# Performance work log

Hardware: AMD Instinct MI355X
Metric: run time of the kernel (lower is better)

Reference implementation:

```python
import jax, jax.numpy as jnp
import numpy as np

B, S, D, H = 128, 512, 256, 512
N_ASSETS = 50
OUT_DIM = N_ASSETS * (N_ASSETS + 1) // 2  # 1275, lower-triangular Cholesky entries


def setup_inputs() -> dict:
    key = jax.random.key(0)
    k = jax.random.split(key, 6)
    x = jax.random.normal(k[0], (B, S, D), dtype=jnp.float32)
    # Layer 0: fused gate weights [D+H, 4H] in gate order (i, f, g, o);
    # equivalent to four separate nn.Linear(D+H, H) layers concatenated.
    W0 = jax.random.normal(k[1], (D + H, 4 * H), jnp.float32) / np.sqrt(D + H)
    b0 = jnp.zeros((4 * H,), jnp.float32).at[H:2 * H].set(1.0)  # forget bias = 1.0
    # Layer 1: input is h of layer 0 -> [H+H, 4H]
    W1 = jax.random.normal(k[2], (2 * H, 4 * H), jnp.float32) / np.sqrt(2 * H)
    b1 = jnp.zeros((4 * H,), jnp.float32).at[H:2 * H].set(1.0)
    Wp = jax.random.normal(k[3], (H, OUT_DIM), jnp.float32) / np.sqrt(H)
    bp = jnp.zeros((OUT_DIM,), jnp.float32)
    return {"x": x, "W0": W0, "b0": b0, "W1": W1, "b1": b1, "Wp": Wp, "bp": bp}


def _cell(xt, h, c, W, b):
    # combined = cat(x, h); single fused GEMM for the 4 gates
    z = jnp.concatenate([xt, h], axis=1) @ W + b  # [B, 4H]
    i, f, g, o = jnp.split(z, 4, axis=1)
    c_new = jax.nn.sigmoid(f) * c + jax.nn.sigmoid(i) * jnp.tanh(g)
    h_new = jax.nn.sigmoid(o) * jnp.tanh(c_new)
    return h_new, c_new


def reference(x, W0, b0, W1, b1, Wp, bp):
    batch = x.shape[0]
    hdim = W0.shape[1] // 4
    init = tuple(jnp.zeros((batch, hdim), x.dtype) for _ in range(4))  # h0,c0,h1,c1

    def step(carry, xt):
        h0, c0, h1, c1 = carry
        h0, c0 = _cell(xt, h0, c0, W0, b0)
        h1, c1 = _cell(h0, h1, c1, W1, b1)
        return (h0, c0, h1, c1), None

    (h0, c0, h1, c1), _ = jax.lax.scan(step, init, jnp.swapaxes(x, 0, 1))
    # Original stacks all timestep outputs but only projects the last hidden state.
    return h1 @ Wp + bp  # [B, OUT_DIM]
```

## Files before the change

kernel.cpp:

```cpp
#include <hip/hip_runtime.h>
#include <stdint.h>

#define BATCH 128
#define SEQ   512
#define DIN   256
#define HID   512
#define NWG   256
#define TPB   512
#define NSLOT 513
#define OUTD  1275
#define HSLOT (BATCH * HID)

#define WS_FLAGS 0
#define WS_H0    4096
#define WS_H1    (4096 + 524288)
#define WS_H1FIN (4096 + 524288 + 262144)
#define WS_XB    (WS_H1FIN + 262144)
#define WS_MSET  (4096 + 524288 + 262144)

typedef __attribute__((ext_vector_type(8))) short bf16x8;
typedef __attribute__((ext_vector_type(4))) unsigned int uint4v;
typedef __attribute__((ext_vector_type(4))) float f32x4;

static __device__ __forceinline__ unsigned short f2bf(float f) {
  unsigned int u = __builtin_bit_cast(unsigned int, f);
  u += 0x7FFFu + ((u >> 16) & 1u);
  return (unsigned short)(u >> 16);
}
static __device__ __forceinline__ float sigmoidf_fast(float v) {
  float e = __expf(-fabsf(v));
  float s = 1.0f / (1.0f + e);
  return v >= 0.0f ? s : 1.0f - s;
}
static __device__ __forceinline__ float tanhf_fast(float v) {
  float e = __expf(-2.0f * fabsf(v));
  float t = (1.0f - e) / (1.0f + e);
  return v >= 0.0f ? t : -t;
}

static __device__ __forceinline__ void ldg_nc(bf16x8& d, const unsigned short* p) {
  asm volatile("global_load_dwordx4 %0, %1, off sc0 sc1" : "=v"(d) : "v"(p));
}
static __device__ __forceinline__ void ldg_nc_dw(unsigned int& d, const unsigned int* p) {
  asm volatile("global_load_dword %0, %1, off sc0 sc1" : "=v"(d) : "v"(p));
}
static __device__ __forceinline__ void stg_nc16(unsigned short* p, uint4v v) {
  asm volatile("global_store_dwordx4 %0, %1, off sc0 sc1" :: "v"(p), "v"(v) : "memory");
}
static __device__ __forceinline__ void stg_nc4(unsigned int* p, unsigned int v) {
  asm volatile("global_store_dword %0, %1, off sc0 sc1" :: "v"(p), "v"(v) : "memory");
}
#define WAIT_TIE1(v) asm volatile("s_waitcnt vmcnt(0)" : "+v"(v) :: "memory")
#define WAIT_TIE4(A)                                                          \
  asm volatile("s_waitcnt vmcnt(0)"                                           \
               : "+v"((A)[0]), "+v"((A)[1]), "+v"((A)[2]), "+v"((A)[3])       \
               :: "memory")
#define WAIT_TIE6(A)                                                          \
  asm volatile("s_waitcnt vmcnt(0)"                                           \
               : "+v"((A)[0]), "+v"((A)[1]), "+v"((A)[2]), "+v"((A)[3]),      \
                 "+v"((A)[4]), "+v"((A)[5]) :: "memory")
#define WAIT_TIE8(A)                                                          \
  asm volatile("s_waitcnt vmcnt(0)"                                           \
               : "+v"((A)[0]), "+v"((A)[1]), "+v"((A)[2]), "+v"((A)[3]),      \
                 "+v"((A)[4]), "+v"((A)[5]), "+v"((A)[6]), "+v"((A)[7])       \
               :: "memory")

static __device__ __forceinline__ int poll_min32(const unsigned int* base, int thr) {
  const unsigned int* fp = base + (threadIdx.x & 31);
  for (;;) {
    unsigned int v;
    ldg_nc_dw(v, fp);
    WAIT_TIE1(v);
    if (__ballot(v >= (unsigned int)thr) == ~0ull) {
      int mn = (int)v;
#pragma unroll
      for (int o = 1; o < 64; o <<= 1) {
        int t = __shfl_xor(mn, o, 64);
        mn = t < mn ? t : mn;
      }
      return mn;
    }
    __builtin_amdgcn_s_sleep(1);
  }
}
static __device__ __forceinline__ int poll_min64(const unsigned int* base, int thr) {
  const unsigned int* fp = base + (threadIdx.x & 63);
  for (;;) {
    unsigned int v;
    ldg_nc_dw(v, fp);
    WAIT_TIE1(v);
    if (__ballot(v >= (unsigned int)thr) == ~0ull) {
      int mn = (int)v;
#pragma unroll
      for (int o = 1; o < 64; o <<= 1) {
        int t = __shfl_xor(mn, o, 64);
        mn = t < mn ? t : mn;
      }
      return mn;
    }
    __builtin_amdgcn_s_sleep(1);
  }
}

__global__ __launch_bounds__(256) void xprep(const float* __restrict__ x,
                                             unsigned short* __restrict__ xb) {
  int p = blockIdx.x;
  int lane = threadIdx.x & 63;
  int g4 = threadIdx.x >> 6;
  int c15 = lane & 15, q = lane >> 4;
  for (int g = 0; g < 16; ++g) {
    int idx = g * 4 + g4;
    int mi = idx >> 3, kt = idx & 7;
    int row = mi * 16 + c15;
    const float* src = x + ((size_t)row * SEQ + p) * DIN + kt * 32 + q * 8;
    f32x4 a = *(const f32x4*)src;
    f32x4 b = *(const f32x4*)(src + 4);
    bf16x8 v;
    v[0] = (short)f2bf(a[0]); v[1] = (short)f2bf(a[1]);
    v[2] = (short)f2bf(a[2]); v[3] = (short)f2bf(a[3]);
    v[4] = (short)f2bf(b[0]); v[5] = (short)f2bf(b[1]);
    v[6] = (short)f2bf(b[2]); v[7] = (short)f2bf(b[3]);
    *(bf16x8*)&xb[((((size_t)p * 8 + mi) * 8 + kt) * 64 + lane) * 8] = v;
  }
}

template <bool USE_XB>
__global__ __launch_bounds__(TPB, 1) void lstm_persistent(
    const float* __restrict__ x, const unsigned short* __restrict__ xb,
    const float* __restrict__ W0, const float* __restrict__ b0,
    const float* __restrict__ W1, const float* __restrict__ b1,
    unsigned int* __restrict__ flags, unsigned short* __restrict__ h0buf,
    unsigned short* __restrict__ h1buf, float* __restrict__ h1fin)
{
  __shared__ unsigned short sWf[4 * 32 * 64 * 8];
  __shared__ float red[4 * 32 * 33];
  __shared__ unsigned short stage[32 * 16];

  const int tid  = threadIdx.x;
  const int wgid = blockIdx.x;
  const int g    = wgid >> 6;
  const int r    = wgid & 63;
  const bool isA = (r < 32);
  const int unit0 = (isA ? r : r - 32) << 4;
  const int lane = tid & 63;
  const int wv   = tid >> 6;
  const int m    = wv & 1;
  const int kq   = wv >> 1;
  const int c15  = lane & 15;
  const int q    = lane >> 4;
  const int miG  = g * 2 + m;
  const int KT   = isA ? 24 : 32;

  {
    const float* W = isA ? W0 : W1;
    for (int f = tid; f < 4 * KT * 64; f += TPB) {
      int ct = f / (KT * 64);
      int rem = f - ct * (KT * 64);
      int kt = rem >> 6, ln = rem & 63;
      int qq = ln >> 4, cc = ln & 15;
      int u_local = ct * 4 + (cc >> 2);
      int gate = cc & 3;
      int gcol = gate * HID + unit0 + u_local;
      int kbase = kt * 32 + qq * 8;
      bf16x8 v;
#pragma unroll
      for (int j = 0; j < 8; ++j)
        v[j] = (short)f2bf(W[(size_t)(kbase + j) * 2048 + gcol]);
      *(bf16x8*)&sWf[(size_t)f * 8] = v;
    }
  }

  const int grow_ = tid >> 3, gu = tid & 7;
  float bias_c[2][4];
  float cst[2] = {0.f, 0.f};
  if (tid < 256) {
    const float* bv = isA ? b0 : b1;
#pragma unroll
    for (int ch = 0; ch < 2; ++ch)
#pragma unroll
      for (int gt = 0; gt < 4; ++gt)
        bias_c[ch][gt] = bv[gt * HID + unit0 + ch * 8 + gu];
  }
  __syncthreads();

  unsigned int* myflags = flags + g * 64;

#define BFRAG(ct, kt) (*(const bf16x8*)&sWf[((((ct) * KT + (kt)) << 6) + lane) << 3])

  int selfSeen = 0, bothSeen = 0, ringSeen = 0;

  for (int p = 0; p < NSLOT; ++p) {
    const unsigned short* h0rd = h0buf + (size_t)((p + 3) & 3) * HSLOT;
    unsigned short* h0wr       = h0buf + (size_t)(p & 3) * HSLOT;
    const unsigned short* h1rd = h1buf + (size_t)(p & 1) * HSLOT;
    unsigned short* h1wr       = h1buf + (size_t)((p + 1) & 1) * HSLOT;
    const bool active = isA ? (p < SEQ) : (p >= 1);

    f32x4 acc[4];
#pragma unroll
    for (int ct = 0; ct < 4; ++ct) acc[ct] = (f32x4){0.f, 0.f, 0.f, 0.f};

    if (isA && active) {
      int ktlo = kq * 6, kthi = ktlo + 6;
      for (int kt = ktlo; kt < kthi && kt < 8; ++kt) {
        bf16x8 ax;
        if (USE_XB) {
          ax = *(const bf16x8*)&xb[((((size_t)p * 8 + miG) * 8 + kt) * 64 + lane) * 8];
        } else {
          const float* xp0 = x + (((size_t)(miG * 16 + c15)) * SEQ + p) * DIN + kt * 32 + q * 8;
          f32x4 a = *(const f32x4*)xp0;
          f32x4 b = *(const f32x4*)(xp0 + 4);
          ax[0] = (short)f2bf(a[0]); ax[1] = (short)f2bf(a[1]);
          ax[2] = (short)f2bf(a[2]); ax[3] = (short)f2bf(a[3]);
          ax[4] = (short)f2bf(b[0]); ax[5] = (short)f2bf(b[1]);
          ax[6] = (short)f2bf(b[2]); ax[7] = (short)f2bf(b[3]);
        }
#pragma unroll
        for (int ct = 0; ct < 4; ++ct)
          acc[ct] = __builtin_amdgcn_mfma_f32_16x16x32_bf16(ax, BFRAG(ct, kt), acc[ct], 0, 0, 0);
      }
    }

    if (wv == 0 && p > 0) {
      if (isA) {
        if (selfSeen < p) selfSeen = poll_min32(myflags, p);
      } else {
        if (bothSeen < p) bothSeen = poll_min64(myflags, p);
      }
    }
    __syncthreads();

    if (active) {
      if (isA) {
        if (kq == 1) {
          bf16x8 ah[4];
#pragma unroll
          for (int i = 0; i < 4; ++i)
            ldg_nc(ah[i], h0rd + ((size_t)(miG * 16 + i) * 64 + lane) * 8);
          WAIT_TIE4(ah);
#pragma unroll
          for (int i = 0; i < 4; ++i)
#pragma unroll
            for (int ct = 0; ct < 4; ++ct)
              acc[ct] = __builtin_amdgcn_mfma_f32_16x16x32_bf16(ah[i], BFRAG(ct, 8 + i), acc[ct], 0, 0, 0);
        } else if (kq >= 2) {
          bf16x8 ah[6];
          int kt0 = kq * 6;
#pragma unroll
          for (int i = 0; i < 6; ++i)
            ldg_nc(ah[i], h0rd + ((size_t)(miG * 16 + (kt0 - 8 + i)) * 64 + lane) * 8);
          WAIT_TIE6(ah);
#pragma unroll
          for (int i = 0; i < 6; ++i)
#pragma unroll
            for (int ct = 0; ct < 4; ++ct)
              acc[ct] = __builtin_amdgcn_mfma_f32_16x16x32_bf16(ah[i], BFRAG(ct, kt0 + i), acc[ct], 0, 0, 0);
        }
      } else {
        bf16x8 ah[8];
        const unsigned short* src = (kq < 2) ? h0rd : h1rd;
        int ktf0 = (kq < 2) ? kq * 8 : (kq - 2) * 8;
#pragma unroll
        for (int i = 0; i < 8; ++i)
          ldg_nc(ah[i], src + ((size_t)(miG * 16 + ktf0 + i) * 64 + lane) * 8);
        WAIT_TIE8(ah);
#pragma unroll
        for (int i = 0; i < 8; ++i)
#pragma unroll
          for (int ct = 0; ct < 4; ++ct)
            acc[ct] = __builtin_amdgcn_mfma_f32_16x16x32_bf16(ah[i], BFRAG(ct, kq * 8 + i), acc[ct], 0, 0, 0);
      }
    }

#pragma unroll
    for (int ch = 0; ch < 2; ++ch) {
      __syncthreads();
      if (active) {
        int lrow = m * 16 + q * 4;
#pragma unroll
        for (int t = 0; t < 2; ++t)
#pragma unroll
          for (int rr = 0; rr < 4; ++rr)
            red[(kq * 32 + lrow + rr) * 33 + t * 16 + c15] = acc[ch * 2 + t][rr];
      }
      __syncthreads();
      if (active && tid < 256) {
        float z[4];
#pragma unroll
        for (int gt = 0; gt < 4; ++gt) {
          float s = bias_c[ch][gt];
          int cidx = gu * 4 + gt;
#pragma unroll
          for (int k2 = 0; k2 < 4; ++k2)
            s += red[(k2 * 32 + grow_) * 33 + cidx];
          z[gt] = s;
        }
        float cn = sigmoidf_fast(z[1]) * cst[ch] + sigmoidf_fast(z[0]) * tanhf_fast(z[2]);
        cst[ch] = cn;
        float hn = sigmoidf_fast(z[3]) * tanhf_fast(cn);
        stage[grow_ * 16 + ch * 8 + gu] = f2bf(hn);
        if (!isA && p == NSLOT - 1)
          h1fin[(size_t)(g * 32 + grow_) * HID + unit0 + ch * 8 + gu] = hn;
      }
    }
    __syncthreads();

    if (wv == 0) {
      if (isA && active && p > 3 && ringSeen < p - 2)
        ringSeen = poll_min32(myflags + 32, p - 2);
      if (active && tid < 64) {
        int row = tid >> 1, qq2 = tid & 1;
        uint4v v = *(const uint4v*)&stage[row * 16 + qq2 * 8];
        int mi = g * 2 + (row >> 4), r15 = row & 15;
        int ktu = unit0 >> 5;
        int qu = ((unit0 & 31) >> 3) + qq2;
        unsigned short* dst = (isA ? h0wr : h1wr) +
            ((size_t)(mi * 16 + ktu) * 64 + qu * 16 + r15) * 8;
        stg_nc16(dst, v);
      }
      asm volatile("s_waitcnt vmcnt(0)" ::: "memory");
      if (tid == 0) stg_nc4(myflags + r, (unsigned int)(p + 1));
    }
  }
#undef BFRAG
}

__global__ __launch_bounds__(256) void proj_kernel(
    const float* __restrict__ h1, const float* __restrict__ Wp,
    const float* __restrict__ bp, float* __restrict__ out)
{
  int o = blockIdx.x * 256 + threadIdx.x;
  int b = blockIdx.y;
  if (o >= OUTD) return;
  const float* hr = h1 + (size_t)b * HID;
  float acc = bp[o];
#pragma unroll 8
  for (int k = 0; k < HID; ++k)
    acc = fmaf(hr[k], Wp[(size_t)k * OUTD + o], acc);
  out[(size_t)b * OUTD + o] = acc;
}

extern "C" void kernel_launch(void* const* d_in, const int* in_sizes, int n_in,
                              void* d_out, int out_size, void* d_ws, size_t ws_size,
                              hipStream_t stream) {
  const float* x  = (const float*)d_in[0];
  const float* W0 = (const float*)d_in[1];
  const float* b0 = (const float*)d_in[2];
  const float* W1 = (const float*)d_in[3];
  const float* b1 = (const float*)d_in[4];
  const float* Wp = (const float*)d_in[5];
  const float* bp = (const float*)d_in[6];
  float* out = (float*)d_out;

  char* ws = (char*)d_ws;
  unsigned int* flags = (unsigned int*)(ws + WS_FLAGS);
  unsigned short* h0b = (unsigned short*)(ws + WS_H0);
  unsigned short* h1b = (unsigned short*)(ws + WS_H1);
  float* h1fin        = (float*)(ws + WS_H1FIN);
  unsigned short* xbp = (unsigned short*)(ws + WS_XB);
  const size_t need_xb = (size_t)WS_XB + (size_t)SEQ * BATCH * DIN * 2;
  const bool use_xb = (ws_size >= need_xb);

  hipMemsetAsync(d_ws, 0, WS_MSET, stream);
  if (use_xb) {
    hipLaunchKernelGGL(xprep, dim3(SEQ), dim3(256), 0, stream, x, xbp);
    hipLaunchKernelGGL(lstm_persistent<true>, dim3(NWG), dim3(TPB), 0, stream,
                       x, xbp, W0, b0, W1, b1, flags, h0b, h1b, h1fin);
  } else {
    hipLaunchKernelGGL(lstm_persistent<false>, dim3(NWG), dim3(TPB), 0, stream,
                       x, xbp, W0, b0, W1, b1, flags, h0b, h1b, h1fin);
  }
  hipLaunchKernelGGL(proj_kernel, dim3((OUTD + 255) / 256, BATCH), dim3(256), 0, stream,
                     h1fin, Wp, bp, out);
}
```

Baseline: 2.919 ms.

## Embed step tags in hidden-state words to replace flag-based synchronization

Hidden states are now stored as fp32 words whose low 10 mantissa bits carry the timestep tag. Consumers poll the data itself (pollcvt) until every word matches the expected step, then convert to bf16, which removes the per-step barrier, LDS staging and flag round-trip. A coarser progress counter still guards ring-buffer reuse. The cost is twice the global traffic for h, spinning on data loads, and slight precision loss from the overwritten mantissa bits.

```diff
diff --git a/kernel.cpp b/kernel.cpp
--- a/kernel.cpp
+++ b/kernel.cpp
@@ -9,17 +9,16 @@
 #define TPB   512
 #define NSLOT 513
 #define OUTD  1275
-#define HSLOT (BATCH * HID)
+#define HSLOTF (BATCH * HID)
 
 #define WS_FLAGS 0
-#define WS_H0    4096
-#define WS_H1    (4096 + 524288)
-#define WS_H1FIN (4096 + 524288 + 262144)
-#define WS_XB    (WS_H1FIN + 262144)
-#define WS_MSET  (4096 + 524288 + 262144)
+#define WS_H0R   4096
+#define WS_H1R   (4096 + 1048576)
+#define WS_H1FIN (4096 + 2097152)
+#define WS_XB    (4096 + 2097152 + 262144)
+#define WS_MSET  (4096 + 2097152)
 
 typedef __attribute__((ext_vector_type(8))) short bf16x8;
-typedef __attribute__((ext_vector_type(4))) unsigned int uint4v;
 typedef __attribute__((ext_vector_type(4))) float f32x4;
 
 static __device__ __forceinline__ unsigned short f2bf(float f) {
@@ -38,51 +37,17 @@
   return v >= 0.0f ? t : -t;
 }
 
-static __device__ __forceinline__ void ldg_nc(bf16x8& d, const unsigned short* p) {
-  asm volatile("global_load_dwordx4 %0, %1, off sc0 sc1" : "=v"(d) : "v"(p));
-}
 static __device__ __forceinline__ void ldg_nc_dw(unsigned int& d, const unsigned int* p) {
   asm volatile("global_load_dword %0, %1, off sc0 sc1" : "=v"(d) : "v"(p));
 }
-static __device__ __forceinline__ void stg_nc16(unsigned short* p, uint4v v) {
-  asm volatile("global_store_dwordx4 %0, %1, off sc0 sc1" :: "v"(p), "v"(v) : "memory");
+static __device__ __forceinline__ void ldg_nc_f4(f32x4& d, const float* p) {
+  asm volatile("global_load_dwordx4 %0, %1, off sc0 sc1" : "=v"(d) : "v"(p));
 }
 static __device__ __forceinline__ void stg_nc4(unsigned int* p, unsigned int v) {
   asm volatile("global_store_dword %0, %1, off sc0 sc1" :: "v"(p), "v"(v) : "memory");
 }
 #define WAIT_TIE1(v) asm volatile("s_waitcnt vmcnt(0)" : "+v"(v) :: "memory")
-#define WAIT_TIE4(A)                                                          \
-  asm volatile("s_waitcnt vmcnt(0)"                                           \
-               : "+v"((A)[0]), "+v"((A)[1]), "+v"((A)[2]), "+v"((A)[3])       \
-               :: "memory")
-#define WAIT_TIE6(A)                                                          \
-  asm volatile("s_waitcnt vmcnt(0)"                                           \
-               : "+v"((A)[0]), "+v"((A)[1]), "+v"((A)[2]), "+v"((A)[3]),      \
-                 "+v"((A)[4]), "+v"((A)[5]) :: "memory")
-#define WAIT_TIE8(A)                                                          \
-  asm volatile("s_waitcnt vmcnt(0)"                                           \
-               : "+v"((A)[0]), "+v"((A)[1]), "+v"((A)[2]), "+v"((A)[3]),      \
-                 "+v"((A)[4]), "+v"((A)[5]), "+v"((A)[6]), "+v"((A)[7])       \
-               :: "memory")
-
-static __device__ __forceinline__ int poll_min32(const unsigned int* base, int thr) {
-  const unsigned int* fp = base + (threadIdx.x & 31);
-  for (;;) {
-    unsigned int v;
-    ldg_nc_dw(v, fp);
-    WAIT_TIE1(v);
-    if (__ballot(v >= (unsigned int)thr) == ~0ull) {
-      int mn = (int)v;
-#pragma unroll
-      for (int o = 1; o < 64; o <<= 1) {
-        int t = __shfl_xor(mn, o, 64);
-        mn = t < mn ? t : mn;
-      }
-      return mn;
-    }
-    __builtin_amdgcn_s_sleep(1);
-  }
-}
+
 static __device__ __forceinline__ int poll_min64(const unsigned int* base, int thr) {
   const unsigned int* fp = base + (threadIdx.x & 63);
   for (;;) {
@@ -92,13 +57,84 @@
     if (__ballot(v >= (unsigned int)thr) == ~0ull) {
       int mn = (int)v;
 #pragma unroll
-      for (int o = 1; o < 64; o <<= 1) {
-        int t = __shfl_xor(mn, o, 64);
-        mn = t < mn ? t : mn;
-      }
+      for (int o = 1; o < 64; o <<= 1) { int t = __shfl_xor(mn, o, 64); mn = t < mn ? t : mn; }
       return mn;
     }
     __builtin_amdgcn_s_sleep(1);
+  }
+}
+
+template <int N>
+static __device__ __forceinline__ void pollcvt(const float* a0, const float* cb,
+                                               unsigned tgt, bf16x8* out) {
+  f32x4 lo[N], hi[N];
+  for (;;) {
+    {
+      unsigned c[N];
+#pragma unroll
+      for (int i = 0; i < N; ++i)
+        ldg_nc_dw(c[i], (const unsigned int*)(cb + (size_t)i * 512));
+      if constexpr (N == 4) {
+        asm volatile("s_waitcnt vmcnt(0)"
+          : "+v"(c[0]), "+v"(c[1]), "+v"(c[2]), "+v"(c[3]) :: "memory");
+      } else if constexpr (N == 6) {
+        asm volatile("s_waitcnt vmcnt(0)"
+          : "+v"(c[0]), "+v"(c[1]), "+v"(c[2]), "+v"(c[3]), "+v"(c[4]), "+v"(c[5])
+          :: "memory");
+      } else {
+        asm volatile("s_waitcnt vmcnt(0)"
+          : "+v"(c[0]), "+v"(c[1]), "+v"(c[2]), "+v"(c[3]),
+            "+v"(c[4]), "+v"(c[5]), "+v"(c[6]), "+v"(c[7]) :: "memory");
+      }
+      unsigned acc = 0;
+#pragma unroll
+      for (int i = 0; i < N; ++i) acc |= c[i] ^ tgt;
+      if (__ballot((acc & 1023u) == 0u) != ~0ull) {
+        __builtin_amdgcn_s_sleep(2);
+        continue;
+      }
+    }
+#pragma unroll
+    for (int i = 0; i < N; ++i) {
+      ldg_nc_f4(lo[i], a0 + (size_t)i * 512);
+      ldg_nc_f4(hi[i], a0 + (size_t)i * 512 + 4);
+    }
+    if constexpr (N == 4) {
+      asm volatile("s_waitcnt vmcnt(0)"
+        : "+v"(lo[0]), "+v"(lo[1]), "+v"(lo[2]), "+v"(lo[3]),
+          "+v"(hi[0]), "+v"(hi[1]), "+v"(hi[2]), "+v"(hi[3]) :: "memory");
+    } else if constexpr (N == 6) {
+      asm volatile("s_waitcnt vmcnt(0)"
+        : "+v"(lo[0]), "+v"(lo[1]), "+v"(lo[2]), "+v"(lo[3]), "+v"(lo[4]), "+v"(lo[5]),
+          "+v"(hi[0]), "+v"(hi[1]), "+v"(hi[2]), "+v"(hi[3]), "+v"(hi[4]), "+v"(hi[5])
+        :: "memory");
+    } else {
+      asm volatile("s_waitcnt vmcnt(0)"
+        : "+v"(lo[0]), "+v"(lo[1]), "+v"(lo[2]), "+v"(lo[3]),
+          "+v"(lo[4]), "+v"(lo[5]), "+v"(lo[6]), "+v"(lo[7]),
+          "+v"(hi[0]), "+v"(hi[1]), "+v"(hi[2]), "+v"(hi[3]),
+          "+v"(hi[4]), "+v"(hi[5]), "+v"(hi[6]), "+v"(hi[7]) :: "memory");
+    }
+    unsigned acc = 0;
+#pragma unroll
+    for (int i = 0; i < N; ++i)
+#pragma unroll
+      for (int j = 0; j < 4; ++j) {
+        acc |= __builtin_bit_cast(unsigned, lo[i][j]) ^ tgt;
+        acc |= __builtin_bit_cast(unsigned, hi[i][j]) ^ tgt;
+      }
+    if (__ballot((acc & 1023u) == 0u) == ~0ull) break;
+    __builtin_amdgcn_s_sleep(1);
+  }
+#pragma unroll
+  for (int i = 0; i < N; ++i) {
+    bf16x8 v;
+#pragma unroll
+    for (int j = 0; j < 4; ++j) {
+      v[j]     = (short)f2bf(lo[i][j]);
+      v[4 + j] = (short)f2bf(hi[i][j]);
+    }
+    out[i] = v;
   }
 }
 
@@ -129,12 +165,11 @@
     const float* __restrict__ x, const unsigned short* __restrict__ xb,
     const float* __restrict__ W0, const float* __restrict__ b0,
     const float* __restrict__ W1, const float* __restrict__ b1,
-    unsigned int* __restrict__ flags, unsigned short* __restrict__ h0buf,
-    unsigned short* __restrict__ h1buf, float* __restrict__ h1fin)
+    unsigned int* __restrict__ prog, float* __restrict__ h0r,
+    float* __restrict__ h1r, float* __restrict__ h1fin)
 {
   __shared__ unsigned short sWf[4 * 32 * 64 * 8];
   __shared__ float red[4 * 32 * 33];
-  __shared__ unsigned short stage[32 * 16];
 
   const int tid  = threadIdx.x;
   const int wgid = blockIdx.x;
@@ -173,32 +208,41 @@
   const int grow_ = tid >> 3, gu = tid & 7;
   float bias_c[2][4];
   float cst[2] = {0.f, 0.f};
+  size_t hoff[2] = {0, 0};
   if (tid < 256) {
     const float* bv = isA ? b0 : b1;
 #pragma unroll
-    for (int ch = 0; ch < 2; ++ch)
+    for (int ch = 0; ch < 2; ++ch) {
 #pragma unroll
       for (int gt = 0; gt < 4; ++gt)
         bias_c[ch][gt] = bv[gt * HID + unit0 + ch * 8 + gu];
+      int U = unit0 + ch * 8 + gu;
+      int mi = g * 2 + (grow_ >> 4), r15g = grow_ & 15;
+      hoff[ch] = ((size_t)(mi * 16 + (U >> 5)) * 64 + ((U & 31) >> 3) * 16 + r15g) * 8 + gu;
+    }
   }
   __syncthreads();
 
-  unsigned int* myflags = flags + g * 64;
+  unsigned int* progF = prog + g * 64;
 
 #define BFRAG(ct, kt) (*(const bf16x8*)&sWf[((((ct) * KT + (kt)) << 6) + lane) << 3])
 
-  int selfSeen = 0, bothSeen = 0, ringSeen = 0;
+  int guardSeen = 0;
 
   for (int p = 0; p < NSLOT; ++p) {
-    const unsigned short* h0rd = h0buf + (size_t)((p + 3) & 3) * HSLOT;
-    unsigned short* h0wr       = h0buf + (size_t)(p & 3) * HSLOT;
-    const unsigned short* h1rd = h1buf + (size_t)(p & 1) * HSLOT;
-    unsigned short* h1wr       = h1buf + (size_t)((p + 1) & 1) * HSLOT;
+    const float* h0rd = h0r + (size_t)((p + 3) & 3) * HSLOTF;
+    float*       h0wr = h0r + (size_t)(p & 3) * HSLOTF;
+    const float* h1rd = h1r + (size_t)((p + 3) & 3) * HSLOTF;
+    float*       h1wr = h1r + (size_t)(p & 3) * HSLOTF;
     const bool active = isA ? (p < SEQ) : (p >= 1);
+    const unsigned tgt = (unsigned)p;
 
     f32x4 acc[4];
 #pragma unroll
     for (int ct = 0; ct < 4; ++ct) acc[ct] = (f32x4){0.f, 0.f, 0.f, 0.f};
+
+    if (wv == 0 && p > 3 && guardSeen < p - 2)
+      guardSeen = poll_min64(progF, p - 2);
 
     if (isA && active) {
       int ktlo = kq * 6, kthi = ktlo + 6;
@@ -221,54 +265,52 @@
       }
     }
 
-    if (wv == 0 && p > 0) {
-      if (isA) {
-        if (selfSeen < p) selfSeen = poll_min32(myflags, p);
-      } else {
-        if (bothSeen < p) bothSeen = poll_min64(myflags, p);
-      }
-    }
-    __syncthreads();
-
     if (active) {
       if (isA) {
-        if (kq == 1) {
+        if (p > 0 && kq == 1) {
           bf16x8 ah[4];
-#pragma unroll
-          for (int i = 0; i < 4; ++i)
-            ldg_nc(ah[i], h0rd + ((size_t)(miG * 16 + i) * 64 + lane) * 8);
-          WAIT_TIE4(ah);
+          const float* a0 = h0rd + ((size_t)(miG * 16 + 0) * 64 + lane) * 8;
+          const float* cb = h0rd + ((size_t)(miG * 16 + 0) * 64 + q * 16) * 8;
+          pollcvt<4>(a0, cb, tgt, ah);
 #pragma unroll
           for (int i = 0; i < 4; ++i)
 #pragma unroll
             for (int ct = 0; ct < 4; ++ct)
               acc[ct] = __builtin_amdgcn_mfma_f32_16x16x32_bf16(ah[i], BFRAG(ct, 8 + i), acc[ct], 0, 0, 0);
-        } else if (kq >= 2) {
+        } else if (p > 0 && kq >= 2) {
           bf16x8 ah[6];
-          int kt0 = kq * 6;
+          int f0 = kq * 6 - 8;
+          const float* a0 = h0rd + ((size_t)(miG * 16 + f0) * 64 + lane) * 8;
+          const float* cb = h0rd + ((size_t)(miG * 16 + f0) * 64 + q * 16) * 8;
+          pollcvt<6>(a0, cb, tgt, ah);
 #pragma unroll
           for (int i = 0; i < 6; ++i)
-            ldg_nc(ah[i], h0rd + ((size_t)(miG * 16 + (kt0 - 8 + i)) * 64 + lane) * 8);
-          WAIT_TIE6(ah);
-#pragma unroll
-          for (int i = 0; i < 6; ++i)
 #pragma unroll
             for (int ct = 0; ct < 4; ++ct)
-              acc[ct] = __builtin_amdgcn_mfma_f32_16x16x32_bf16(ah[i], BFRAG(ct, kt0 + i), acc[ct], 0, 0, 0);
+              acc[ct] = __builtin_amdgcn_mfma_f32_16x16x32_bf16(ah[i], BFRAG(ct, kq * 6 + i), acc[ct], 0, 0, 0);
         }
       } else {
-        bf16x8 ah[8];
-        const unsigned short* src = (kq < 2) ? h0rd : h1rd;
-        int ktf0 = (kq < 2) ? kq * 8 : (kq - 2) * 8;
-#pragma unroll
-        for (int i = 0; i < 8; ++i)
-          ldg_nc(ah[i], src + ((size_t)(miG * 16 + ktf0 + i) * 64 + lane) * 8);
-        WAIT_TIE8(ah);
-#pragma unroll
-        for (int i = 0; i < 8; ++i)
-#pragma unroll
-          for (int ct = 0; ct < 4; ++ct)
-            acc[ct] = __builtin_amdgcn_mfma_f32_16x16x32_bf16(ah[i], BFRAG(ct, kq * 8 + i), acc[ct], 0, 0, 0);
+        if (kq < 2) {
+          bf16x8 ah[8];
+          const float* a0 = h0rd + ((size_t)(miG * 16 + kq * 8) * 64 + lane) * 8;
+          const float* cb = h0rd + ((size_t)(miG * 16 + kq * 8) * 64 + q * 16) * 8;
+          pollcvt<8>(a0, cb, tgt, ah);
+#pragma unroll
+          for (int i = 0; i < 8; ++i)
+#pragma unroll
+            for (int ct = 0; ct < 4; ++ct)
+              acc[ct] = __builtin_amdgcn_mfma_f32_16x16x32_bf16(ah[i], BFRAG(ct, kq * 8 + i), acc[ct], 0, 0, 0);
+        } else if (p > 1) {
+          bf16x8 ah[8];
+          const float* a0 = h1rd + ((size_t)(miG * 16 + (kq - 2) * 8) * 64 + lane) * 8;
+          const float* cb = h1rd + ((size_t)(miG * 16 + (kq - 2) * 8) * 64 + q * 16) * 8;
+          pollcvt<8>(a0, cb, tgt, ah);
+#pragma unroll
+          for (int i = 0; i < 8; ++i)
+#pragma unroll
+            for (int ct = 0; ct < 4; ++ct)
+              acc[ct] = __builtin_amdgcn_mfma_f32_16x16x32_bf16(ah[i], BFRAG(ct, kq * 8 + i), acc[ct], 0, 0, 0);
+        }
       }
     }
 
@@ -298,29 +340,14 @@
         float cn = sigmoidf_fast(z[1]) * cst[ch] + sigmoidf_fast(z[0]) * tanhf_fast(z[2]);
         cst[ch] = cn;
         float hn = sigmoidf_fast(z[3]) * tanhf_fast(cn);
-        stage[grow_ * 16 + ch * 8 + gu] = f2bf(hn);
+        unsigned hb = (__builtin_bit_cast(unsigned, hn) & ~1023u) | (unsigned)(p + 1);
+        stg_nc4((unsigned int*)((isA ? h0wr : h1wr) + hoff[ch]), hb);
         if (!isA && p == NSLOT - 1)
           h1fin[(size_t)(g * 32 + grow_) * HID + unit0 + ch * 8 + gu] = hn;
       }
     }
-    __syncthreads();
-
-    if (wv == 0) {
-      if (isA && active && p > 3 && ringSeen < p - 2)
-        ringSeen = poll_min32(myflags + 32, p - 2);
-      if (active && tid < 64) {
-        int row = tid >> 1, qq2 = tid & 1;
-        uint4v v = *(const uint4v*)&stage[row * 16 + qq2 * 8];
-        int mi = g * 2 + (row >> 4), r15 = row & 15;
-        int ktu = unit0 >> 5;
-        int qu = ((unit0 & 31) >> 3) + qq2;
-        unsigned short* dst = (isA ? h0wr : h1wr) +
-            ((size_t)(mi * 16 + ktu) * 64 + qu * 16 + r15) * 8;
-        stg_nc16(dst, v);
-      }
-      asm volatile("s_waitcnt vmcnt(0)" ::: "memory");
-      if (tid == 0) stg_nc4(myflags + r, (unsigned int)(p + 1));
-    }
+
+    if (tid == 0) stg_nc4(progF + r, (unsigned int)(p + 1));
   }
 #undef BFRAG
 }
@@ -353,9 +380,9 @@
   float* out = (float*)d_out;
 
   char* ws = (char*)d_ws;
-  unsigned int* flags = (unsigned int*)(ws + WS_FLAGS);
-  unsigned short* h0b = (unsigned short*)(ws + WS_H0);
-  unsigned short* h1b = (unsigned short*)(ws + WS_H1);
+  unsigned int* prog  = (unsigned int*)(ws + WS_FLAGS);
+  float* h0r          = (float*)(ws + WS_H0R);
+  float* h1r          = (float*)(ws + WS_H1R);
   float* h1fin        = (float*)(ws + WS_H1FIN);
   unsigned short* xbp = (unsigned short*)(ws + WS_XB);
   const size_t need_xb = (size_t)WS_XB + (size_t)SEQ * BATCH * DIN * 2;
@@ -365,10 +392,10 @@
   if (use_xb) {
     hipLaunchKernelGGL(xprep, dim3(SEQ), dim3(256), 0, stream, x, xbp);
     hipLaunchKernelGGL(lstm_persistent<true>, dim3(NWG), dim3(TPB), 0, stream,
-                       x, xbp, W0, b0, W1, b1, flags, h0b, h1b, h1fin);
+                       x, xbp, W0, b0, W1, b1, prog, h0r, h1r, h1fin);
   } else {
     hipLaunchKernelGGL(lstm_persistent<false>, dim3(NWG), dim3(TPB), 0, stream,
-                       x, xbp, W0, b0, W1, b1, flags, h0b, h1b, h1fin);
+                       x, xbp, W0, b0, W1, b1, prog, h0r, h1r, h1fin);
   }
   hipLaunchKernelGGL(proj_kernel, dim3((OUTD + 255) / 256, BATCH), dim3(256), 0, stream,
                      h1fin, Wp, bp, out);
```

New measurement: 3.052 ms. 4.5% more time.
